# Kernel tuning notes

Hardware: AMD Instinct MI355X
Metric: run time of the kernel (lower is better)

Reference implementation:

```python
import jax, jax.numpy as jnp
import numpy as np

B, L, E, MODES = 32, 2048, 512, 32  # batch, seq_len, d_model, kept Fourier modes (mode_select='low')


def setup_inputs() -> dict:
    key = jax.random.key(0)
    ks = jax.random.split(key, 6)
    scale = 1.0 / (E * E)  # FourierBlock scale = 1/(in_channels*out_channels), torch.rand init
    lin = E ** -0.5
    return {
        "queries": jax.random.normal(ks[0], (B, L, E), jnp.float32),
        "Wq": jax.random.normal(ks[1], (E, E), jnp.float32) * lin,
        "bq": jnp.zeros((E,), jnp.float32),
        "W1r": jax.random.uniform(ks[2], (E, E, MODES), jnp.float32) * scale,
        "W1i": jax.random.uniform(ks[3], (E, E, MODES), jnp.float32) * scale,
        "Wo": jax.random.normal(ks[4], (E, E), jnp.float32) * lin,
        "bo": jnp.zeros((E,), jnp.float32),
    }


def reference(queries, Wq, bq, W1r, W1i, Wo, bo):
    Bn, Ln, En = queries.shape
    # query projection
    q = queries @ Wq.T + bq                                    # (B, L, E)
    # FourierBlock: FFT along time, keep low `MODES` bins, complex channel mixing, inverse FFT
    xf = jnp.fft.rfft(q, axis=1)                               # (B, L//2+1, E) complex64
    W1 = (W1r + 1j * W1i).astype(jnp.complex64)                # (E_in, E_out, M)
    sel = xf[:, :MODES, :]                                     # (B, M, E) selected modes (mode_select='low')
    out_sel = jnp.einsum('bmi,iom->bmo', sel, W1)              # per-mode complex E x E mixing
    nfreq = Ln // 2 + 1
    out_ft = jnp.zeros((Bn, nfreq, En), jnp.complex64).at[:, :MODES, :].set(out_sel)
    x = jnp.fft.irfft(out_ft, n=Ln, axis=1)                    # (B, L, E) real
    # output projection (attn is None in the original; return the tensor output)
    return x @ Wo.T + bo
```

## Files before the change

kernel.cpp:

```cpp
#include <hip/hip_runtime.h>
#include <hip/hip_bf16.h>

typedef _Float16 f16;
typedef _Float16 f16x8 __attribute__((ext_vector_type(8)));
typedef _Float16 f16x4 __attribute__((ext_vector_type(4)));
typedef float f32x4 __attribute__((ext_vector_type(4)));

#define QPAD 136
#define PADK2 72

#define W1SCALE 262144.0f
#define W1DESCALE 3.814697265625e-06f

static __device__ __forceinline__ f32x4 mfma16(f16x8 a, f16x8 b, f32x4 c) {
  return __builtin_amdgcn_mfma_f32_16x16x32_f16(a, b, c, 0, 0, 0);
}

__global__ __launch_bounds__(256) void k_prep(f16* __restrict__ FhT, f16* __restrict__ Gh,
                                              const float* __restrict__ Wq,
                                              const float* __restrict__ Wo,
                                              f16* __restrict__ Wq16,
                                              f16* __restrict__ Wo16) {
  int idx = blockIdx.x * 256 + threadIdx.x;
  const float w = 6.28318530717958647692f / 2048.0f;
  {
    int k2 = idx >> 11, l = idx & 2047;
    int k = k2 & 31;
    float th = (float)((k * l) & 2047) * w;
    float v = (k2 < 32) ? cosf(th) : -sinf(th);
    FhT[k2 * 2048 + l] = (f16)v;
  }
  {
    int l = idx >> 6, kk = idx & 63;
    int k = kk & 31;
    float th = (float)((k * l) & 2047) * w;
    float v;
    if (kk < 32) v = ((k == 0) ? 1.0f : 2.0f) * (1.0f / 2048.0f) * cosf(th);
    else         v = (k == 0) ? 0.0f : (-2.0f / 2048.0f) * sinf(th);
    Gh[l * 64 + kk] = (f16)v;
  }
  {
    const float* src = (idx < 65536) ? Wq : Wo;
    f16* dst = (idx < 65536) ? Wq16 : Wo16;
    int i = idx & 65535;
    float4 v = ((const float4*)src)[i];
    f16x4 o = {(f16)v.x, (f16)v.y, (f16)v.z, (f16)v.w};
    *(f16x4*)(dst + (size_t)i * 4) = o;
  }
}

__global__ __launch_bounds__(256) void k_dft_fwd(const f16* __restrict__ FhT,
                                                 const float* __restrict__ queries,
                                                 float* __restrict__ p32) {
  __shared__ __align__(16) f16 As[64 * QPAD];
  __shared__ __align__(16) f16 Bs[64 * QPAD];
  const int n0 = blockIdx.x * 64;
  const int b  = blockIdx.y;
  const int kb = blockIdx.z * 512;
  const int t = threadIdx.x;
  const int wid = t >> 6, lane = t & 63;
  const int mh = wid & 1, nh = wid >> 1;
  const int l15 = lane & 15, kq = lane >> 4;
  const int arow = t >> 2, ac0 = (t & 3) << 5;
  const int bcol = t & 63, bkg = t >> 6;
  f32x4 acc[2][2] = {};
  for (int ph = 0; ph < 4; ++ph) {
    const int k0 = kb + ph * 128;
    __syncthreads();
#pragma unroll
    for (int j = 0; j < 4; ++j)
      *(f16x8*)(As + arow * QPAD + ac0 + j * 8) =
          *(const f16x8*)(FhT + (size_t)arow * 2048 + k0 + ac0 + j * 8);
    const float* qp = queries + ((size_t)b * 2048 + k0 + bkg * 32) * 512 + n0 + bcol;
    float v[32];
#pragma unroll
    for (int r = 0; r < 32; ++r) v[r] = qp[(size_t)r * 512];
#pragma unroll
    for (int s = 0; s < 4; ++s) {
      f16x8 pk = {(f16)v[s*8+0], (f16)v[s*8+1], (f16)v[s*8+2], (f16)v[s*8+3],
                  (f16)v[s*8+4], (f16)v[s*8+5], (f16)v[s*8+6], (f16)v[s*8+7]};
      *(f16x8*)(Bs + bcol * QPAD + bkg * 32 + s * 8) = pk;
    }
    __syncthreads();
#pragma unroll
    for (int ks = 0; ks < 4; ++ks) {
      const int kofs = ks * 32 + kq * 8;
      f16x8 a0 = *(const f16x8*)(As + (mh * 32 + 0  + l15) * QPAD + kofs);
      f16x8 a1 = *(const f16x8*)(As + (mh * 32 + 16 + l15) * QPAD + kofs);
      f16x8 b0 = *(const f16x8*)(Bs + (nh * 32 + 0  + l15) * QPAD + kofs);
      f16x8 b1 = *(const f16x8*)(Bs + (nh * 32 + 16 + l15) * QPAD + kofs);
      acc[0][0] = mfma16(a0, b0, acc[0][0]);
      acc[0][1] = mfma16(a0, b1, acc[0][1]);
      acc[1][0] = mfma16(a1, b0, acc[1][0]);
      acc[1][1] = mfma16(a1, b1, acc[1][1]);
    }
  }
#pragma unroll
  for (int mf = 0; mf < 2; ++mf)
#pragma unroll
    for (int nf = 0; nf < 2; ++nf)
#pragma unroll
      for (int r = 0; r < 4; ++r) {
        int k2 = mh * 32 + mf * 16 + kq * 4 + r;
        int col = n0 + nh * 32 + nf * 16 + l15;
        p32[((size_t)blockIdx.z * 2048 + b * 64 + k2) * 512 + col] = acc[mf][nf][r];
      }
}

__global__ __launch_bounds__(256) void k_reduceN(const float* __restrict__ p,
                                                 f16* __restrict__ dst, int ns) {
  size_t i4 = (size_t)blockIdx.x * 256 + threadIdx.x;
  float4 s = {0.f, 0.f, 0.f, 0.f};
  for (int c = 0; c < ns; ++c) {
    float4 v = ((const float4*)p)[(size_t)c * 262144 + i4];
    s.x += v.x; s.y += v.y; s.z += v.z; s.w += v.w;
  }
  f16x4 o = {(f16)s.x, (f16)s.y, (f16)s.z, (f16)s.w};
  *(f16x4*)(dst + i4 * 4) = o;
}

__global__ __launch_bounds__(256) void k_gemm_nk(const f16* __restrict__ A,
                                                 const f16* __restrict__ Bnk,
                                                 f16* __restrict__ C,
                                                 const float* __restrict__ bias0,
                                                 float bscale, int selt) {
  __shared__ __align__(16) f16 As[64 * QPAD];
  __shared__ __align__(16) f16 Bs[32 * QPAD];
  const int n0 = blockIdx.x * 32, m0 = blockIdx.y * 64;
  const int t = threadIdx.x;
  const int wid = t >> 6, lane = t & 63;
  const int mh = wid & 1, nh = wid >> 1;
  const int l15 = lane & 15, kq = lane >> 4;
  const int row = t >> 2, c0 = (t & 3) << 5;
  f32x4 acc[2] = {};
  for (int ph = 0; ph < 4; ++ph) {
    const int k0 = ph * 128;
    __syncthreads();
#pragma unroll
    for (int j = 0; j < 4; ++j)
      *(f16x8*)(As + row * QPAD + c0 + j * 8) =
          *(const f16x8*)(A + (size_t)(m0 + row) * 512 + k0 + c0 + j * 8);
    if (t < 128) {
      const int br = t >> 2, bc0 = (t & 3) << 5;
#pragma unroll
      for (int j = 0; j < 4; ++j)
        *(f16x8*)(Bs + br * QPAD + bc0 + j * 8) =
            *(const f16x8*)(Bnk + (size_t)(n0 + br) * 512 + k0 + bc0 + j * 8);
    }
    __syncthreads();
#pragma unroll
    for (int ks = 0; ks < 4; ++ks) {
      const int kofs = ks * 32 + kq * 8;
      f16x8 a0 = *(const f16x8*)(As + (mh * 32 + 0  + l15) * QPAD + kofs);
      f16x8 a1 = *(const f16x8*)(As + (mh * 32 + 16 + l15) * QPAD + kofs);
      f16x8 b0 = *(const f16x8*)(Bs + (nh * 16 + l15) * QPAD + kofs);
      acc[0] = mfma16(a0, b0, acc[0]);
      acc[1] = mfma16(a1, b0, acc[1]);
    }
  }
#pragma unroll
  for (int mf = 0; mf < 2; ++mf)
#pragma unroll
    for (int r = 0; r < 4; ++r) {
      int mg = m0 + mh * 32 + mf * 16 + kq * 4 + r;
      int col = n0 + nh * 16 + l15;
      float cv = acc[mf][r];
      if (bias0 != nullptr && (mg & 63) == 0) cv += bscale * bias0[col];
      size_t didx = selt ? (((size_t)(mg & 63) * 32 + (mg >> 6)) * 512 + col)
                         : ((size_t)mg * 512 + col);
      C[didx] = (f16)cv;
    }
}

__global__ __launch_bounds__(512) void k_modes_fused(const float* __restrict__ W1r,
                                                     const float* __restrict__ W1i,
                                                     const f16* __restrict__ selT,
                                                     float* __restrict__ pmode) {
  __shared__ __align__(16) f16 Wst[2][16][648];
  const int o0 = blockIdx.x * 16, m0 = blockIdx.y * 16, is = blockIdx.z;
  const int t = threadIdx.x;
  const int lane = t & 63, wv = t >> 6;
  const int l15 = lane & 15, kq = lane >> 4, kofs = kq << 3;
  const int mq = t & 3, p = t >> 2;
  const int soo = p & 15, sib = p >> 4;
  f32x4 accR[2][2] = {}, accI[2][2] = {};
  const int ibase = is * 128;
  for (int ch = 0; ch < 4; ++ch) {
    const int i0c = ibase + ch * 32;
    __syncthreads();
#pragma unroll
    for (int ri = 0; ri < 2; ++ri) {
      const float* src = ri ? W1i : W1r;
#pragma unroll
      for (int qq = 0; qq < 4; ++qq) {
        int ii = sib + 8 * qq;
        const float4 v = *(const float4*)(src + (size_t)(i0c + ii) * 16384 +
                                          (o0 + soo) * 32 + m0 + mq * 4);
        f16* wp = &Wst[ri][mq * 4][soo * 40 + ii];
        wp[0 * 648] = (f16)(W1SCALE * v.x);
        wp[1 * 648] = (f16)(W1SCALE * v.y);
        wp[2 * 648] = (f16)(W1SCALE * v.z);
        wp[3 * 648] = (f16)(W1SCALE * v.w);
      }
    }
    __syncthreads();
#pragma unroll
    for (int ml = 0; ml < 2; ++ml) {
      const int mloc = 2 * wv + ml;
      const int mg = m0 + mloc;
      f16x8 ar0 = *(const f16x8*)(selT + ((size_t)mg * 32 + 0  + l15) * 512 + i0c + kofs);
      f16x8 ar1 = *(const f16x8*)(selT + ((size_t)mg * 32 + 16 + l15) * 512 + i0c + kofs);
      f16x8 ai0 = *(const f16x8*)(selT + ((size_t)(32 + mg) * 32 + 0  + l15) * 512 + i0c + kofs);
      f16x8 ai1 = *(const f16x8*)(selT + ((size_t)(32 + mg) * 32 + 16 + l15) * 512 + i0c + kofs);
      f16x8 br = *(const f16x8*)(&Wst[0][mloc][l15 * 40 + kofs]);
      f16x8 bi = *(const f16x8*)(&Wst[1][mloc][l15 * 40 + kofs]);
      f16x8 ain0 = -ai0, ain1 = -ai1;
      accR[ml][0] = mfma16(ar0,  br, accR[ml][0]);
      accR[ml][0] = mfma16(ain0, bi, accR[ml][0]);
      accI[ml][0] = mfma16(ar0,  bi, accI[ml][0]);
      accI[ml][0] = mfma16(ai0,  br, accI[ml][0]);
      accR[ml][1] = mfma16(ar1,  br, accR[ml][1]);
      accR[ml][1] = mfma16(ain1, bi, accR[ml][1]);
      accI[ml][1] = mfma16(ar1,  bi, accI[ml][1]);
      accI[ml][1] = mfma16(ai1,  br, accI[ml][1]);
    }
  }
#pragma unroll
  for (int ml = 0; ml < 2; ++ml) {
    const int mg = m0 + 2 * wv + ml;
#pragma unroll
    for (int bt = 0; bt < 2; ++bt)
#pragma unroll
      for (int r = 0; r < 4; ++r) {
        int bb = bt * 16 + kq * 4 + r;
        int og = o0 + l15;
        pmode[((size_t)is * 2048 + bb * 64 + mg) * 512 + og]      = accR[ml][bt][r];
        pmode[((size_t)is * 2048 + bb * 64 + 32 + mg) * 512 + og] = accI[ml][bt][r];
      }
  }
}

__global__ __launch_bounds__(256) void k_dft_inv(const f16* __restrict__ Gh,
                                                 const f16* __restrict__ u,
                                                 const float* __restrict__ bo,
                                                 float* __restrict__ out) {
  __shared__ __align__(16) f16 As[64 * PADK2];
  __shared__ __align__(16) f16 Bs[64 * PADK2];
  const int n0 = blockIdx.x * 64, l0 = blockIdx.y * 64, b = blockIdx.z;
  const int t = threadIdx.x, wid = t >> 6, lane = t & 63;
  const int mh = wid & 1, nh = wid >> 1;
#pragma unroll
  for (int p = 0; p < 2; ++p) {
    int v = t + 256 * p, row = v >> 3, c8 = (v & 7) << 3;
    *(f16x8*)(As + row * PADK2 + c8) = *(const f16x8*)(Gh + (size_t)(l0 + row) * 64 + c8);
  }
  {
    int col = t & 63, kg = t >> 6;
    const f16* up = u + ((size_t)b * 64 + kg * 16) * 512 + n0 + col;
    f16 vv[16];
#pragma unroll
    for (int s = 0; s < 16; ++s) vv[s] = up[(size_t)s * 512];
#pragma unroll
    for (int s4 = 0; s4 < 4; ++s4) {
      f16x4 pk = {vv[s4 * 4], vv[s4 * 4 + 1], vv[s4 * 4 + 2], vv[s4 * 4 + 3]};
      *(f16x4*)(Bs + col * PADK2 + kg * 16 + s4 * 4) = pk;
    }
  }
  __syncthreads();
  f32x4 acc[2][2] = {};
#pragma unroll
  for (int ks = 0; ks < 2; ++ks) {
    const int kofs = ks * 32 + ((lane >> 4) << 3);
    f16x8 a0 = *(const f16x8*)(As + (mh * 32 + 0  + (lane & 15)) * PADK2 + kofs);
    f16x8 a1 = *(const f16x8*)(As + (mh * 32 + 16 + (lane & 15)) * PADK2 + kofs);
    f16x8 b0 = *(const f16x8*)(Bs + (nh * 32 + 0  + (lane & 15)) * PADK2 + kofs);
    f16x8 b1 = *(const f16x8*)(Bs + (nh * 32 + 16 + (lane & 15)) * PADK2 + kofs);
    acc[0][0] = mfma16(a0, b0, acc[0][0]);
    acc[0][1] = mfma16(a0, b1, acc[0][1]);
    acc[1][0] = mfma16(a1, b0, acc[1][0]);
    acc[1][1] = mfma16(a1, b1, acc[1][1]);
  }
#pragma unroll
  for (int mf = 0; mf < 2; ++mf)
#pragma unroll
    for (int nf = 0; nf < 2; ++nf)
#pragma unroll
      for (int r = 0; r < 4; ++r) {
        int l = l0 + mh * 32 + mf * 16 + ((lane >> 4) << 2) + r;
        int col = n0 + nh * 32 + nf * 16 + (lane & 15);
        float cv = acc[mf][nf][r] * W1DESCALE + bo[col];
        out[((size_t)b * 2048 + l) * 512 + col] = cv;
      }
}

extern "C" void kernel_launch(void* const* d_in, const int* in_sizes, int n_in,
                              void* d_out, int out_size, void* d_ws, size_t ws_size,
                              hipStream_t stream) {
  const float* queries = (const float*)d_in[0];
  const float* Wq      = (const float*)d_in[1];
  const float* bq      = (const float*)d_in[2];
  const float* W1r     = (const float*)d_in[3];
  const float* W1i     = (const float*)d_in[4];
  const float* Wo      = (const float*)d_in[5];
  const float* bo      = (const float*)d_in[6];
  float* out           = (float*)d_out;

  char* ws = (char*)d_ws;
  size_t off = 0;
  auto alloc = [&](size_t bytes) {
    off = (off + 255) & ~(size_t)255;
    char* p = ws + off;
    off += bytes;
    return p;
  };
  f16* FhT    = (f16*)alloc((size_t)64 * 2048 * 2);
  f16* Gh     = (f16*)alloc((size_t)2048 * 64 * 2);
  f16* Wq16   = (f16*)alloc((size_t)512 * 512 * 2);
  f16* Wo16   = (f16*)alloc((size_t)512 * 512 * 2);
  float* p32  = (float*)alloc((size_t)4 * 2048 * 512 * 4);
  f16* t16    = (f16*)alloc((size_t)2048 * 512 * 2);
  f16* selT   = (f16*)alloc((size_t)2048 * 512 * 2);
  float* pmode= (float*)alloc((size_t)4 * 2048 * 512 * 4);
  f16* osel   = (f16*)alloc((size_t)2048 * 512 * 2);
  f16* u16    = (f16*)alloc((size_t)2048 * 512 * 2);

  hipLaunchKernelGGL(k_prep, dim3(512), dim3(256), 0, stream, FhT, Gh, Wq, Wo, Wq16, Wo16);
  hipLaunchKernelGGL(k_dft_fwd, dim3(8, 32, 4), dim3(256), 0, stream, FhT, queries, p32);
  hipLaunchKernelGGL(k_reduceN, dim3(1024), dim3(256), 0, stream, p32, t16, 4);
  hipLaunchKernelGGL(k_gemm_nk, dim3(16, 32), dim3(256), 0, stream, t16, Wq16, selT,
                     bq, 2048.0f, 1);
  hipLaunchKernelGGL(k_modes_fused, dim3(32, 2, 4), dim3(512), 0, stream,
                     W1r, W1i, selT, pmode);
  hipLaunchKernelGGL(k_reduceN, dim3(1024), dim3(256), 0, stream, pmode, osel, 4);
  hipLaunchKernelGGL(k_gemm_nk, dim3(16, 32), dim3(256), 0, stream, osel, Wo16, u16,
                     (const float*)nullptr, 0.0f, 0);
  hipLaunchKernelGGL(k_dft_inv, dim3(8, 32, 32), dim3(256), 0, stream, Gh, u16, bo, out);
}
```

Baseline: 126.5 us.

## Fuse split-K partial reduction into GEMM loads, store partials in fp16

Both split-K partial buffers (forward DFT and mode mixing) are now written as fp16 instead of fp32. The standalone reduce kernels are removed, and the following GEMM sums the partials while it loads its A tile. The mode-mixing kernel's input-channel split goes from 4 to 8 slices, giving more blocks for the W1-bandwidth-bound stage. This drops two launches and halves partial traffic, but the A tile of each GEMM is re-read once per column block, and summing partials in fp16 adds rounding error.

```diff
diff --git a/kernel.cpp b/kernel.cpp
--- a/kernel.cpp
+++ b/kernel.cpp
@@ -51,7 +51,7 @@
 
 __global__ __launch_bounds__(256) void k_dft_fwd(const f16* __restrict__ FhT,
                                                  const float* __restrict__ queries,
-                                                 float* __restrict__ p32) {
+                                                 f16* __restrict__ p16) {
   __shared__ __align__(16) f16 As[64 * QPAD];
   __shared__ __align__(16) f16 Bs[64 * QPAD];
   const int n0 = blockIdx.x * 64;
@@ -103,27 +103,15 @@
       for (int r = 0; r < 4; ++r) {
         int k2 = mh * 32 + mf * 16 + kq * 4 + r;
         int col = n0 + nh * 32 + nf * 16 + l15;
-        p32[((size_t)blockIdx.z * 2048 + b * 64 + k2) * 512 + col] = acc[mf][nf][r];
+        p16[((size_t)blockIdx.z * 2048 + b * 64 + k2) * 512 + col] = (f16)acc[mf][nf][r];
       }
 }
 
-__global__ __launch_bounds__(256) void k_reduceN(const float* __restrict__ p,
-                                                 f16* __restrict__ dst, int ns) {
-  size_t i4 = (size_t)blockIdx.x * 256 + threadIdx.x;
-  float4 s = {0.f, 0.f, 0.f, 0.f};
-  for (int c = 0; c < ns; ++c) {
-    float4 v = ((const float4*)p)[(size_t)c * 262144 + i4];
-    s.x += v.x; s.y += v.y; s.z += v.z; s.w += v.w;
-  }
-  f16x4 o = {(f16)s.x, (f16)s.y, (f16)s.z, (f16)s.w};
-  *(f16x4*)(dst + i4 * 4) = o;
-}
-
-__global__ __launch_bounds__(256) void k_gemm_nk(const f16* __restrict__ A,
-                                                 const f16* __restrict__ Bnk,
-                                                 f16* __restrict__ C,
-                                                 const float* __restrict__ bias0,
-                                                 float bscale, int selt) {
+__global__ __launch_bounds__(256) void k_gemm_red(const f16* __restrict__ P, int np,
+                                                  const f16* __restrict__ Bnk,
+                                                  f16* __restrict__ C,
+                                                  const float* __restrict__ bias0,
+                                                  float bscale, int selt) {
   __shared__ __align__(16) f16 As[64 * QPAD];
   __shared__ __align__(16) f16 Bs[32 * QPAD];
   const int n0 = blockIdx.x * 32, m0 = blockIdx.y * 64;
@@ -137,9 +125,13 @@
     const int k0 = ph * 128;
     __syncthreads();
 #pragma unroll
-    for (int j = 0; j < 4; ++j)
-      *(f16x8*)(As + row * QPAD + c0 + j * 8) =
-          *(const f16x8*)(A + (size_t)(m0 + row) * 512 + k0 + c0 + j * 8);
+    for (int j = 0; j < 4; ++j) {
+      size_t aidx = (size_t)(m0 + row) * 512 + k0 + c0 + j * 8;
+      f16x8 s = *(const f16x8*)(P + aidx);
+      for (int c = 1; c < np; ++c)
+        s = s + *(const f16x8*)(P + (size_t)c * 1048576 + aidx);
+      *(f16x8*)(As + row * QPAD + c0 + j * 8) = s;
+    }
     if (t < 128) {
       const int br = t >> 2, bc0 = (t & 3) << 5;
 #pragma unroll
@@ -175,7 +167,7 @@
 __global__ __launch_bounds__(512) void k_modes_fused(const float* __restrict__ W1r,
                                                      const float* __restrict__ W1i,
                                                      const f16* __restrict__ selT,
-                                                     float* __restrict__ pmode) {
+                                                     f16* __restrict__ pmode) {
   __shared__ __align__(16) f16 Wst[2][16][648];
   const int o0 = blockIdx.x * 16, m0 = blockIdx.y * 16, is = blockIdx.z;
   const int t = threadIdx.x;
@@ -184,8 +176,8 @@
   const int mq = t & 3, p = t >> 2;
   const int soo = p & 15, sib = p >> 4;
   f32x4 accR[2][2] = {}, accI[2][2] = {};
-  const int ibase = is * 128;
-  for (int ch = 0; ch < 4; ++ch) {
+  const int ibase = is * 64;
+  for (int ch = 0; ch < 2; ++ch) {
     const int i0c = ibase + ch * 32;
     __syncthreads();
 #pragma unroll
@@ -234,8 +226,8 @@
       for (int r = 0; r < 4; ++r) {
         int bb = bt * 16 + kq * 4 + r;
         int og = o0 + l15;
-        pmode[((size_t)is * 2048 + bb * 64 + mg) * 512 + og]      = accR[ml][bt][r];
-        pmode[((size_t)is * 2048 + bb * 64 + 32 + mg) * 512 + og] = accI[ml][bt][r];
+        pmode[((size_t)is * 2048 + bb * 64 + mg) * 512 + og]      = (f16)accR[ml][bt][r];
+        pmode[((size_t)is * 2048 + bb * 64 + 32 + mg) * 512 + og] = (f16)accI[ml][bt][r];
       }
   }
 }
@@ -317,22 +309,18 @@
   f16* Gh     = (f16*)alloc((size_t)2048 * 64 * 2);
   f16* Wq16   = (f16*)alloc((size_t)512 * 512 * 2);
   f16* Wo16   = (f16*)alloc((size_t)512 * 512 * 2);
-  float* p32  = (float*)alloc((size_t)4 * 2048 * 512 * 4);
-  f16* t16    = (f16*)alloc((size_t)2048 * 512 * 2);
+  f16* p16    = (f16*)alloc((size_t)4 * 2048 * 512 * 2);
   f16* selT   = (f16*)alloc((size_t)2048 * 512 * 2);
-  float* pmode= (float*)alloc((size_t)4 * 2048 * 512 * 4);
-  f16* osel   = (f16*)alloc((size_t)2048 * 512 * 2);
+  f16* pmode  = (f16*)alloc((size_t)8 * 2048 * 512 * 2);
   f16* u16    = (f16*)alloc((size_t)2048 * 512 * 2);
 
   hipLaunchKernelGGL(k_prep, dim3(512), dim3(256), 0, stream, FhT, Gh, Wq, Wo, Wq16, Wo16);
-  hipLaunchKernelGGL(k_dft_fwd, dim3(8, 32, 4), dim3(256), 0, stream, FhT, queries, p32);
-  hipLaunchKernelGGL(k_reduceN, dim3(1024), dim3(256), 0, stream, p32, t16, 4);
-  hipLaunchKernelGGL(k_gemm_nk, dim3(16, 32), dim3(256), 0, stream, t16, Wq16, selT,
+  hipLaunchKernelGGL(k_dft_fwd, dim3(8, 32, 4), dim3(256), 0, stream, FhT, queries, p16);
+  hipLaunchKernelGGL(k_gemm_red, dim3(16, 32), dim3(256), 0, stream, p16, 4, Wq16, selT,
                      bq, 2048.0f, 1);
-  hipLaunchKernelGGL(k_modes_fused, dim3(32, 2, 4), dim3(512), 0, stream,
+  hipLaunchKernelGGL(k_modes_fused, dim3(32, 2, 8), dim3(512), 0, stream,
                      W1r, W1i, selT, pmode);
-  hipLaunchKernelGGL(k_reduceN, dim3(1024), dim3(256), 0, stream, pmode, osel, 4);
-  hipLaunchKernelGGL(k_gemm_nk, dim3(16, 32), dim3(256), 0, stream, osel, Wo16, u16,
+  hipLaunchKernelGGL(k_gemm_red, dim3(16, 32), dim3(256), 0, stream, pmode, 8, Wo16, u16,
                      (const float*)nullptr, 0.0f, 0);
   hipLaunchKernelGGL(k_dft_inv, dim3(8, 32, 32), dim3(256), 0, stream, Gh, u16, bo, out);
 }
```

Result: slower. 170.5 us (+34.8%).
